# Performance work log

Measured on AMD Instinct MI355X. Metric: run time of the kernel, lower is better.

## Reference

```python
import jax, jax.numpy as jnp
import numpy as np

E = 16        # n_routed_experts
TOP_K = 2
C = 768       # n_embd
I = 1536      # intermediate_size
B, T = 8, 2048


def setup_inputs() -> dict:
    key = jax.random.key(0)
    ks = jax.random.split(key, 9)
    s = 0.02  # init scale
    return {
        "x": jax.random.normal(ks[0], (B, T, C), jnp.float32),
        "w_gate": jax.random.normal(ks[1], (C, E), jnp.float32) * s,
        "expert_bias": jnp.zeros((E,), jnp.float32),
        "wg": jax.random.normal(ks[2], (E, C, I), jnp.float32) * s,
        "wu": jax.random.normal(ks[3], (E, C, I), jnp.float32) * s,
        "wd": jax.random.normal(ks[4], (E, I, C), jnp.float32) * s,
        "swg": jax.random.normal(ks[5], (C, I), jnp.float32) * s,
        "swu": jax.random.normal(ks[6], (C, I), jnp.float32) * s,
        "swd": jax.random.normal(ks[7], (I, C), jnp.float32) * s,
    }


def _expert(x, wg_e, wu_e, wd_e):
    # SwiGLU FFN: down(silu(gate(x)) * up(x))
    return (jax.nn.silu(x @ wg_e) * (x @ wu_e)) @ wd_e


def reference(x, w_gate, expert_bias, wg, wu, wd, swg, swu, swd):
    Bq, Tq, Cq = x.shape
    xf = x.reshape(-1, Cq)  # (N, C)
    n_tok = xf.shape[0]

    # shared experts (1 expert, divided by count=1)
    shared = _expert(xf, swg, swu, swd)

    # router: softmax over (logits + bias), top-k, renormalize
    logits = xf @ w_gate + expert_bias  # (N, E)
    probs = jax.nn.softmax(logits, axis=-1)
    topk_p, topk_i = jax.lax.top_k(probs, TOP_K)
    topk_p = topk_p / jnp.sum(topk_p, axis=-1, keepdims=True)

    # combine weights per expert: zero where expert not selected
    comb = jnp.zeros((n_tok, E), xf.dtype).at[
        jnp.arange(n_tok)[:, None], topk_i
    ].add(topk_p)  # (N, E)

    routed = jnp.zeros_like(xf)
    for e in range(E):  # fixed small expert count
        routed = routed + comb[:, e:e + 1] * _expert(xf, wg[e], wu[e], wd[e])

    return (shared + routed).reshape(Bq, Tq, Cq)
```

## Files before the change

### kernel.cpp

```cpp
#include <hip/hip_runtime.h>

typedef unsigned short u16;
typedef unsigned int u32;
typedef __attribute__((ext_vector_type(4))) float f32x4;
typedef __attribute__((ext_vector_type(8))) short short8;
typedef __attribute__((ext_vector_type(4))) u16 u16x4;

#define N_TOK 16384
#define C_DIM 768
#define I_DIM 1536
#define N_EXP 16
#define TM 128
#define BK 64
#define LSTR 80
#define MAXT 400

#define CI_COUNTS 0
#define CI_STARTS 32
#define CI_NTILES 64
#define CI_TILE_E 128
#define CI_TILE_R 640
#define CI_ESLOT 2048
#define CI_SLOT 34816
#define CI_TOKW 67584
#define CI_PERM 100352

#define XB_OFF  (1u << 20)
#define ACT_OFF 26214400u
#define Y_OFF   183500800u

__device__ __forceinline__ u16 f2bf(float f) {
  u32 x = __float_as_uint(f);
  return (u16)((x + 0x7FFFu + ((x >> 16) & 1u)) >> 16);
}
__device__ __forceinline__ float bf2f(u16 h) {
  return __uint_as_float(((u32)h) << 16);
}

__global__ void router_kernel(const float* __restrict__ x, const float* __restrict__ wgate,
                              const float* __restrict__ ebias, int* __restrict__ ctrl,
                              u16* __restrict__ xb) {
  __shared__ float xs[16 * 772];
  __shared__ float wgs[C_DIM * 16];
  __shared__ float lg[16 * 16];
  int tid = threadIdx.x;
  int tok0 = blockIdx.x * 16;
  const float4* xsrc = (const float4*)(x + (size_t)tok0 * C_DIM);
  const float4* wsrc = (const float4*)wgate;
  float4* wdst = (float4*)wgs;
#pragma unroll
  for (int j = 0; j < 12; j++) {
    int q = tid + j * 256;
    float4 v = xsrc[q];
    int tk = q / 192;
    int c4 = q - tk * 192;
    *(float4*)&xs[tk * 772 + c4 * 4] = v;
    u16x4 o; o.x = f2bf(v.x); o.y = f2bf(v.y); o.z = f2bf(v.z); o.w = f2bf(v.w);
    *(u16x4*)(xb + (size_t)tok0 * C_DIM + (size_t)q * 4) = o;
    wdst[q] = wsrc[q];
  }
  __syncthreads();
  int tk = tid >> 4, e = tid & 15;
  float acc = ebias[e];
  const float* xrow = &xs[tk * 772];
  for (int c = 0; c < C_DIM; c++) acc = fmaf(xrow[c], wgs[c * 16 + e], acc);
  lg[tk * 16 + e] = acc;
  __syncthreads();
  if (tid < 16) {
    int n = tok0 + tid;
    float l0 = -1e30f, l1 = -1e30f; int i0 = 0, i1 = 0;
#pragma unroll
    for (int j = 0; j < 16; j++) {
      float l = lg[tid * 16 + j];
      if (l > l0) { l1 = l0; i1 = i0; l0 = l; i0 = j; }
      else if (l > l1) { l1 = l; i1 = j; }
    }
    float e1 = __expf(l1 - l0);
    float inv = 1.f / (1.f + e1);
    int s0 = atomicAdd(&ctrl[CI_COUNTS + i0], 1);
    int s1 = atomicAdd(&ctrl[CI_COUNTS + i1], 1);
    ctrl[CI_ESLOT + 2 * n]     = (i0 << 24) | s0;
    ctrl[CI_ESLOT + 2 * n + 1] = (i1 << 24) | s1;
    float* tw = (float*)(ctrl + CI_TOKW);
    tw[2 * n] = inv; tw[2 * n + 1] = e1 * inv;
  }
}

__global__ void tiles_kernel(int* __restrict__ ctrl) {
  if (threadIdx.x != 0) return;
  int cnt[17];
#pragma unroll
  for (int e = 0; e < 16; e++) cnt[e] = ctrl[CI_COUNTS + e];
  cnt[16] = N_TOK;
  ctrl[CI_COUNTS + 16] = N_TOK;
  int cur = 0, T = 0;
  for (int e = 0; e <= 16; e++) {
    ctrl[CI_STARTS + e] = cur;
    int nt = (cnt[e] + TM - 1) >> 7;
    for (int i = 0; i < nt; i++) {
      ctrl[CI_TILE_E + T] = e;
      ctrl[CI_TILE_R + T] = cur + i * TM;
      T++;
    }
    cur += nt << 7;
  }
  ctrl[CI_NTILES] = T;
}

__global__ void scatter_kernel(int* __restrict__ ctrl) {
  int n = blockIdx.x * 256 + threadIdx.x;
#pragma unroll
  for (int k = 0; k < 2; k++) {
    int es = ctrl[CI_ESLOT + 2 * n + k];
    int e = es >> 24;
    int slot = es & 0xFFFFFF;
    int row = ctrl[CI_STARTS + e] + slot;
    ctrl[CI_PERM + row] = n;
    ctrl[CI_SLOT + 2 * n + k] = row;
  }
}

__global__ __launch_bounds__(256, 2)
void gemm1_kernel(const u16* __restrict__ xb, const float* __restrict__ wg,
                  const float* __restrict__ wu, const float* __restrict__ swg,
                  const float* __restrict__ swu, u16* __restrict__ act,
                  const int* __restrict__ ctrl) {
  __shared__ u16 Al[TM * LSTR];
  __shared__ u16 Bg[TM * LSTR];
  __shared__ u16 Bu[TM * LSTR];
  int t = blockIdx.x;
  if (t >= ctrl[CI_NTILES]) return;
  int e = ctrl[CI_TILE_E + t];
  int row0 = ctrl[CI_TILE_R + t];
  int col0 = blockIdx.y * TM;
  int seg_start = ctrl[CI_STARTS + e];
  bool sh = (e == N_EXP);
  const float* G; const float* U;
  if (sh) { G = swg; U = swu; }
  else { G = wg + (size_t)e * C_DIM * I_DIM; U = wu + (size_t)e * C_DIM * I_DIM; }
  int row_lim = sh ? 0x7fffffff : (seg_start + ctrl[CI_COUNTS + e]);
  const int* perm = ctrl + CI_PERM;
  int tid = threadIdx.x;
  int tok[4];
#pragma unroll
  for (int j = 0; j < 4; j++) {
    int r_loc = (tid + j * 256) >> 3;
    int r = row0 + r_loc;
    tok[j] = sh ? (r - seg_start) : ((r < row_lim) ? perm[r] : 0);
  }
  f32x4 accg[4][4], accu[4][4];
#pragma unroll
  for (int m = 0; m < 4; m++)
#pragma unroll
    for (int n = 0; n < 4; n++) {
      f32x4 z = {0.f, 0.f, 0.f, 0.f};
      accg[m][n] = z; accu[m][n] = z;
    }
  int lane = tid & 63, wv = tid >> 6;
  int rh = (wv & 1) * 64, chh = (wv >> 1) * 64;
  int lr = lane & 15, lq = lane >> 4;

  for (int kk = 0; kk < C_DIM; kk += BK) {
#pragma unroll
    for (int j = 0; j < 4; j++) {
      int ch = tid + j * 256;
      int r_loc = ch >> 3;
      int c = ch & 7;
      int p = c ^ (r_loc & 7);
      float4 v = *(const float4*)(xb + (size_t)tok[j] * C_DIM + kk + c * 8);
      *(float4*)&Al[r_loc * LSTR + p * 8] = v;
    }
#pragma unroll 2
    for (int j = 0; j < 8; j++) {
      int u = tid + j * 256;
      int i = u & 127;
      int k4 = u >> 7;
      size_t gb = (size_t)(kk + k4 * 4) * I_DIM + col0 + i;
      float g0 = G[gb], g1 = G[gb + I_DIM], g2 = G[gb + 2 * I_DIM], g3 = G[gb + 3 * I_DIM];
      float h0 = U[gb], h1 = U[gb + I_DIM], h2 = U[gb + 2 * I_DIM], h3 = U[gb + 3 * I_DIM];
      int off = i * LSTR + (((k4 >> 1) ^ (i & 7)) * 8) + (k4 & 1) * 4;
      u16x4 pg; pg.x = f2bf(g0); pg.y = f2bf(g1); pg.z = f2bf(g2); pg.w = f2bf(g3);
      u16x4 pu; pu.x = f2bf(h0); pu.y = f2bf(h1); pu.z = f2bf(h2); pu.w = f2bf(h3);
      *(u16x4*)&Bg[off] = pg;
      *(u16x4*)&Bu[off] = pu;
    }
    __syncthreads();
#pragma unroll
    for (int s = 0; s < 2; s++) {
      int cidx = s * 4 + lq;
      short8 af[4], bg_[4], bu_[4];
#pragma unroll
      for (int m = 0; m < 4; m++) {
        int r = rh + m * 16 + lr;
        af[m] = *(const short8*)&Al[r * LSTR + ((cidx ^ (r & 7)) * 8)];
      }
#pragma unroll
      for (int n = 0; n < 4; n++) {
        int i = chh + n * 16 + lr;
        int off = i * LSTR + ((cidx ^ (i & 7)) * 8);
        bg_[n] = *(const short8*)&Bg[off];
        bu_[n] = *(const short8*)&Bu[off];
      }
#pragma unroll
      for (int m = 0; m < 4; m++)
#pragma unroll
        for (int n = 0; n < 4; n++) {
          accg[m][n] = __builtin_amdgcn_mfma_f32_16x16x32_bf16(af[m], bg_[n], accg[m][n], 0, 0, 0);
          accu[m][n] = __builtin_amdgcn_mfma_f32_16x16x32_bf16(af[m], bu_[n], accu[m][n], 0, 0, 0);
        }
    }
    __syncthreads();
  }
#pragma unroll
  for (int m = 0; m < 4; m++)
#pragma unroll
    for (int n = 0; n < 4; n++)
#pragma unroll
      for (int rg = 0; rg < 4; rg++) {
        float g = accg[m][n][rg];
        float h = accu[m][n][rg];
        float a = g * (1.f / (1.f + __expf(-g))) * h;
        int r_loc = rh + m * 16 + lq * 4 + rg;
        int cl = col0 + chh + n * 16 + lr;
        act[(size_t)(row0 + r_loc) * I_DIM + cl] = f2bf(a);
      }
}

__global__ __launch_bounds__(256, 2)
void gemm2_kernel(const u16* __restrict__ act, const float* __restrict__ wd,
                  const float* __restrict__ swd, u16* __restrict__ y,
                  const int* __restrict__ ctrl) {
  __shared__ u16 Al[TM * LSTR];
  __shared__ u16 Bl[TM * LSTR];
  int t = blockIdx.x;
  if (t >= ctrl[CI_NTILES]) return;
  int e = ctrl[CI_TILE_E + t];
  int row0 = ctrl[CI_TILE_R + t];
  int col0 = blockIdx.y * TM;
  const float* D = (e == N_EXP) ? swd : (wd + (size_t)e * I_DIM * C_DIM);
  int tid = threadIdx.x;
  f32x4 acc[4][4];
#pragma unroll
  for (int m = 0; m < 4; m++)
#pragma unroll
    for (int n = 0; n < 4; n++) {
      f32x4 z = {0.f, 0.f, 0.f, 0.f};
      acc[m][n] = z;
    }
  int lane = tid & 63, wv = tid >> 6;
  int rh = (wv & 1) * 64, chh = (wv >> 1) * 64;
  int lr = lane & 15, lq = lane >> 4;

  for (int kk = 0; kk < I_DIM; kk += BK) {
#pragma unroll
    for (int j = 0; j < 4; j++) {
      int ch = tid + j * 256;
      int r_loc = ch >> 3;
      int c = ch & 7;
      int p = c ^ (r_loc & 7);
      float4 v = *(const float4*)(act + (size_t)(row0 + r_loc) * I_DIM + kk + c * 8);
      *(float4*)&Al[r_loc * LSTR + p * 8] = v;
    }
#pragma unroll 2
    for (int j = 0; j < 8; j++) {
      int u = tid + j * 256;
      int i = u & 127;
      int k4 = u >> 7;
      size_t gb = (size_t)(kk + k4 * 4) * C_DIM + col0 + i;
      float g0 = D[gb], g1 = D[gb + C_DIM], g2 = D[gb + 2 * C_DIM], g3 = D[gb + 3 * C_DIM];
      int off = i * LSTR + (((k4 >> 1) ^ (i & 7)) * 8) + (k4 & 1) * 4;
      u16x4 pg; pg.x = f2bf(g0); pg.y = f2bf(g1); pg.z = f2bf(g2); pg.w = f2bf(g3);
      *(u16x4*)&Bl[off] = pg;
    }
    __syncthreads();
#pragma unroll
    for (int s = 0; s < 2; s++) {
      int cidx = s * 4 + lq;
      short8 af[4], bf_[4];
#pragma unroll
      for (int m = 0; m < 4; m++) {
        int r = rh + m * 16 + lr;
        af[m] = *(const short8*)&Al[r * LSTR + ((cidx ^ (r & 7)) * 8)];
      }
#pragma unroll
      for (int n = 0; n < 4; n++) {
        int i = chh + n * 16 + lr;
        bf_[n] = *(const short8*)&Bl[i * LSTR + ((cidx ^ (i & 7)) * 8)];
      }
#pragma unroll
      for (int m = 0; m < 4; m++)
#pragma unroll
        for (int n = 0; n < 4; n++)
          acc[m][n] = __builtin_amdgcn_mfma_f32_16x16x32_bf16(af[m], bf_[n], acc[m][n], 0, 0, 0);
    }
    __syncthreads();
  }
#pragma unroll
  for (int m = 0; m < 4; m++)
#pragma unroll
    for (int n = 0; n < 4; n++)
#pragma unroll
      for (int rg = 0; rg < 4; rg++) {
        int r_loc = rh + m * 16 + lq * 4 + rg;
        int cl = col0 + chh + n * 16 + lr;
        y[(size_t)(row0 + r_loc) * C_DIM + cl] = f2bf(acc[m][n][rg]);
      }
}

__global__ void combine_kernel(const u16* __restrict__ y, const int* __restrict__ ctrl,
                               float* __restrict__ out) {
  int idx = blockIdx.x * 256 + threadIdx.x;
  int n = idx / 192;
  int c = (idx - n * 192) * 4;
  int srow = ctrl[CI_STARTS + 16] + n;
  int s0 = ctrl[CI_SLOT + 2 * n];
  int s1 = ctrl[CI_SLOT + 2 * n + 1];
  const float* tw = (const float*)(ctrl + CI_TOKW);
  float w0 = tw[2 * n], w1 = tw[2 * n + 1];
  u16x4 a = *(const u16x4*)(y + (size_t)srow * C_DIM + c);
  u16x4 b = *(const u16x4*)(y + (size_t)s0 * C_DIM + c);
  u16x4 d = *(const u16x4*)(y + (size_t)s1 * C_DIM + c);
  float4 o;
  o.x = bf2f(a.x) + w0 * bf2f(b.x) + w1 * bf2f(d.x);
  o.y = bf2f(a.y) + w0 * bf2f(b.y) + w1 * bf2f(d.y);
  o.z = bf2f(a.z) + w0 * bf2f(b.z) + w1 * bf2f(d.z);
  o.w = bf2f(a.w) + w0 * bf2f(b.w) + w1 * bf2f(d.w);
  *(float4*)(out + (size_t)idx * 4) = o;
}

extern "C" void kernel_launch(void* const* d_in, const int* in_sizes, int n_in,
                              void* d_out, int out_size, void* d_ws, size_t ws_size,
                              hipStream_t stream) {
  (void)in_sizes; (void)n_in; (void)out_size; (void)ws_size;
  const float* x     = (const float*)d_in[0];
  const float* wgate = (const float*)d_in[1];
  const float* ebias = (const float*)d_in[2];
  const float* wg    = (const float*)d_in[3];
  const float* wu    = (const float*)d_in[4];
  const float* wd    = (const float*)d_in[5];
  const float* swg   = (const float*)d_in[6];
  const float* swu   = (const float*)d_in[7];
  const float* swd   = (const float*)d_in[8];
  float* out = (float*)d_out;
  char* ws = (char*)d_ws;
  int* ctrl = (int*)ws;
  u16* xb  = (u16*)(ws + XB_OFF);
  u16* act = (u16*)(ws + ACT_OFF);
  u16* y   = (u16*)(ws + Y_OFF);

  hipMemsetAsync(ws, 0, 256, stream);
  router_kernel<<<N_TOK / 16, 256, 0, stream>>>(x, wgate, ebias, ctrl, xb);
  tiles_kernel<<<1, 64, 0, stream>>>(ctrl);
  scatter_kernel<<<N_TOK / 256, 256, 0, stream>>>(ctrl);
  gemm1_kernel<<<dim3(MAXT, I_DIM / TM), 256, 0, stream>>>(xb, wg, wu, swg, swu, act, ctrl);
  gemm2_kernel<<<dim3(MAXT, C_DIM / TM), 256, 0, stream>>>(act, wd, swd, y, ctrl);
  combine_kernel<<<(N_TOK * C_DIM / 4) / 256, 256, 0, stream>>>(y, ctrl, out);
}
```

Measured before the change: 1.181 ms.

## Pre-convert weights to bf16, DMA tiles into LDS, fuse combine via atomics

A new convert kernel transposes and converts all expert and shared weights to bf16 once per call. The GEMMs then load A and B tiles straight into LDS with global_load_lds 16-byte DMA instead of doing per-element fp32 loads and conversion in registers. gemm2 scatters weighted results directly into the output with atomicAdd, which removes the y buffer and the combine kernel. The GEMMs run in two passes so the act buffer is smaller and may stay cache-resident, and the router gets a transposed, vectorized dot product. In exchange it adds a full weight-conversion pass on every call, output memsets, and many fp32 atomics, and the atomics make the summation order nondeterministic.

```diff
diff --git a/kernel.cpp b/kernel.cpp
--- a/kernel.cpp
+++ b/kernel.cpp
@@ -5,6 +5,7 @@
 typedef __attribute__((ext_vector_type(4))) float f32x4;
 typedef __attribute__((ext_vector_type(8))) short short8;
 typedef __attribute__((ext_vector_type(4))) u16 u16x4;
+typedef __attribute__((ext_vector_type(8))) u16 u16x8;
 
 #define N_TOK 16384
 #define C_DIM 768
@@ -12,22 +13,22 @@
 #define N_EXP 16
 #define TM 128
 #define BK 64
-#define LSTR 80
 #define MAXT 400
+#define PASS_T 200
 
 #define CI_COUNTS 0
 #define CI_STARTS 32
 #define CI_NTILES 64
 #define CI_TILE_E 128
-#define CI_TILE_R 640
 #define CI_ESLOT 2048
-#define CI_SLOT 34816
-#define CI_TOKW 67584
-#define CI_PERM 100352
-
-#define XB_OFF  (1u << 20)
-#define ACT_OFF 26214400u
-#define Y_OFF   183500800u
+#define CI_TOKW 36864
+#define CI_PERM 102400
+#define CI_RW 153600
+
+#define XB_OFF  1048576u
+#define WGU_OFF 26214400u
+#define WDP_OFF 106430464u
+#define ACT_OFF 146538496u
 
 __device__ __forceinline__ u16 f2bf(float f) {
   u32 x = __float_as_uint(f);
@@ -35,19 +36,57 @@
 }
 __device__ __forceinline__ float bf2f(u16 h) {
   return __uint_as_float(((u32)h) << 16);
+}
+__device__ __forceinline__ void dma16(const void* g, void* l) {
+  __builtin_amdgcn_global_load_lds(
+      (const __attribute__((address_space(1))) unsigned int*)g,
+      (__attribute__((address_space(3))) unsigned int*)l, 16, 0, 0);
+}
+
+__global__ void convert_kernel(const float* __restrict__ wg, const float* __restrict__ wu,
+                               const float* __restrict__ wd, const float* __restrict__ swg,
+                               const float* __restrict__ swu, const float* __restrict__ swd,
+                               u16* __restrict__ wgu, u16* __restrict__ wdp) {
+  int bid = blockIdx.x;
+  const float* src; u16* dst; int K, N, base_n;
+  if (bid < 34 * 48) {
+    int m = bid / 48, nb = bid % 48;
+    int e = m >> 1, gu = m & 1;
+    src = (e < N_EXP) ? ((gu ? wu : wg) + (size_t)e * C_DIM * I_DIM) : (gu ? swu : swg);
+    dst = wgu + (size_t)m * (C_DIM * I_DIM);
+    K = C_DIM; N = I_DIM; base_n = nb * 32;
+  } else {
+    int b2 = bid - 34 * 48;
+    int e = b2 / 24, nb = b2 % 24;
+    src = (e < N_EXP) ? (wd + (size_t)e * I_DIM * C_DIM) : swd;
+    dst = wdp + (size_t)e * (I_DIM * C_DIM);
+    K = I_DIM; N = C_DIM; base_n = nb * 32;
+  }
+  int tid = threadIdx.x, lane = tid & 63, wv = tid >> 6;
+  int lsub = lane >> 3, lchk = lane & 7;
+  int ng = base_n + wv * 8 + lsub;
+  int c = lchk ^ (ng & 7);
+  const float* s0 = src + ng;
+  u16* drow = dst + (size_t)ng * K;
+  for (int k0 = 0; k0 < K; k0 += 64) {
+    u16x8 o;
+#pragma unroll
+    for (int j = 0; j < 8; j++)
+      o[j] = f2bf(s0[(size_t)(k0 + c * 8 + j) * N]);
+    *(u16x8*)&drow[k0 + lchk * 8] = o;
+  }
 }
 
 __global__ void router_kernel(const float* __restrict__ x, const float* __restrict__ wgate,
                               const float* __restrict__ ebias, int* __restrict__ ctrl,
                               u16* __restrict__ xb) {
   __shared__ float xs[16 * 772];
-  __shared__ float wgs[C_DIM * 16];
+  __shared__ float wgsT[16 * 772];
   __shared__ float lg[16 * 16];
   int tid = threadIdx.x;
   int tok0 = blockIdx.x * 16;
   const float4* xsrc = (const float4*)(x + (size_t)tok0 * C_DIM);
   const float4* wsrc = (const float4*)wgate;
-  float4* wdst = (float4*)wgs;
 #pragma unroll
   for (int j = 0; j < 12; j++) {
     int q = tid + j * 256;
@@ -57,13 +96,23 @@
     *(float4*)&xs[tk * 772 + c4 * 4] = v;
     u16x4 o; o.x = f2bf(v.x); o.y = f2bf(v.y); o.z = f2bf(v.z); o.w = f2bf(v.w);
     *(u16x4*)(xb + (size_t)tok0 * C_DIM + (size_t)q * 4) = o;
-    wdst[q] = wsrc[q];
+    float4 w = wsrc[q];
+    int c = q >> 2, e0 = (q & 3) * 4;
+    wgsT[(e0 + 0) * 772 + c] = w.x;
+    wgsT[(e0 + 1) * 772 + c] = w.y;
+    wgsT[(e0 + 2) * 772 + c] = w.z;
+    wgsT[(e0 + 3) * 772 + c] = w.w;
   }
   __syncthreads();
   int tk = tid >> 4, e = tid & 15;
   float acc = ebias[e];
-  const float* xrow = &xs[tk * 772];
-  for (int c = 0; c < C_DIM; c++) acc = fmaf(xrow[c], wgs[c * 16 + e], acc);
+  const float4* xr = (const float4*)&xs[tk * 772];
+  const float4* wr = (const float4*)&wgsT[e * 772];
+#pragma unroll 4
+  for (int c4 = 0; c4 < 192; c4++) {
+    float4 xv = xr[c4], wv = wr[c4];
+    acc = fmaf(xv.x, wv.x, fmaf(xv.y, wv.y, fmaf(xv.z, wv.z, fmaf(xv.w, wv.w, acc))));
+  }
   lg[tk * 16 + e] = acc;
   __syncthreads();
   if (tid < 16) {
@@ -97,11 +146,7 @@
   for (int e = 0; e <= 16; e++) {
     ctrl[CI_STARTS + e] = cur;
     int nt = (cnt[e] + TM - 1) >> 7;
-    for (int i = 0; i < nt; i++) {
-      ctrl[CI_TILE_E + T] = e;
-      ctrl[CI_TILE_R + T] = cur + i * TM;
-      T++;
-    }
+    for (int i = 0; i < nt; i++) ctrl[CI_TILE_E + T++] = e;
     cur += nt << 7;
   }
   ctrl[CI_NTILES] = T;
@@ -109,6 +154,8 @@
 
 __global__ void scatter_kernel(int* __restrict__ ctrl) {
   int n = blockIdx.x * 256 + threadIdx.x;
+  const float* tw = (const float*)(ctrl + CI_TOKW);
+  float* rw = (float*)(ctrl + CI_RW);
 #pragma unroll
   for (int k = 0; k < 2; k++) {
     int es = ctrl[CI_ESLOT + 2 * n + k];
@@ -116,38 +163,46 @@
     int slot = es & 0xFFFFFF;
     int row = ctrl[CI_STARTS + e] + slot;
     ctrl[CI_PERM + row] = n;
-    ctrl[CI_SLOT + 2 * n + k] = row;
-  }
+    rw[row] = tw[2 * n + k];
+  }
+  int srow = ctrl[CI_STARTS + 16] + n;
+  ctrl[CI_PERM + srow] = n;
+  rw[srow] = 1.0f;
 }
 
 __global__ __launch_bounds__(256, 2)
-void gemm1_kernel(const u16* __restrict__ xb, const float* __restrict__ wg,
-                  const float* __restrict__ wu, const float* __restrict__ swg,
-                  const float* __restrict__ swu, u16* __restrict__ act,
-                  const int* __restrict__ ctrl) {
-  __shared__ u16 Al[TM * LSTR];
-  __shared__ u16 Bg[TM * LSTR];
-  __shared__ u16 Bu[TM * LSTR];
-  int t = blockIdx.x;
+void gemm1_kernel(const u16* __restrict__ xb, const u16* __restrict__ wgu,
+                  u16* __restrict__ act, const int* __restrict__ ctrl, int tile0) {
+  __shared__ u16 Al[TM * BK];
+  __shared__ u16 Bg[TM * BK];
+  __shared__ u16 Bu[TM * BK];
+  int t = tile0 + blockIdx.x;
   if (t >= ctrl[CI_NTILES]) return;
   int e = ctrl[CI_TILE_E + t];
-  int row0 = ctrl[CI_TILE_R + t];
+  int row0 = t << 7;
+  int row0l = blockIdx.x << 7;
   int col0 = blockIdx.y * TM;
   int seg_start = ctrl[CI_STARTS + e];
   bool sh = (e == N_EXP);
-  const float* G; const float* U;
-  if (sh) { G = swg; U = swu; }
-  else { G = wg + (size_t)e * C_DIM * I_DIM; U = wu + (size_t)e * C_DIM * I_DIM; }
+  const u16* G = wgu + (size_t)(2 * e) * (C_DIM * I_DIM);
+  const u16* U = G + C_DIM * I_DIM;
   int row_lim = sh ? 0x7fffffff : (seg_start + ctrl[CI_COUNTS + e]);
   const int* perm = ctrl + CI_PERM;
   int tid = threadIdx.x;
-  int tok[4];
+  int lane = tid & 63, wv = tid >> 6;
+  int lsub = lane >> 3;
+  int lchk = lane & 7;
+  int co = (lchk ^ lsub) * 8;
+  const u16* aptr[4];
 #pragma unroll
   for (int j = 0; j < 4; j++) {
-    int r_loc = (tid + j * 256) >> 3;
-    int r = row0 + r_loc;
-    tok[j] = sh ? (r - seg_start) : ((r < row_lim) ? perm[r] : 0);
-  }
+    int r = row0 + wv * 32 + j * 8 + lsub;
+    int tok = sh ? (r - seg_start) : ((r < row_lim) ? perm[r] : 0);
+    aptr[j] = xb + (size_t)tok * C_DIM + co;
+  }
+  size_t boff = (size_t)(col0 + wv * 32 + lsub) * C_DIM + lchk * 8;
+  int ldst = wv * 2048;
+
   f32x4 accg[4][4], accu[4][4];
 #pragma unroll
   for (int m = 0; m < 4; m++)
@@ -156,33 +211,15 @@
       f32x4 z = {0.f, 0.f, 0.f, 0.f};
       accg[m][n] = z; accu[m][n] = z;
     }
-  int lane = tid & 63, wv = tid >> 6;
+  int lr = lane & 15, lq = lane >> 4;
   int rh = (wv & 1) * 64, chh = (wv >> 1) * 64;
-  int lr = lane & 15, lq = lane >> 4;
 
   for (int kk = 0; kk < C_DIM; kk += BK) {
 #pragma unroll
     for (int j = 0; j < 4; j++) {
-      int ch = tid + j * 256;
-      int r_loc = ch >> 3;
-      int c = ch & 7;
-      int p = c ^ (r_loc & 7);
-      float4 v = *(const float4*)(xb + (size_t)tok[j] * C_DIM + kk + c * 8);
-      *(float4*)&Al[r_loc * LSTR + p * 8] = v;
-    }
-#pragma unroll 2
-    for (int j = 0; j < 8; j++) {
-      int u = tid + j * 256;
-      int i = u & 127;
-      int k4 = u >> 7;
-      size_t gb = (size_t)(kk + k4 * 4) * I_DIM + col0 + i;
-      float g0 = G[gb], g1 = G[gb + I_DIM], g2 = G[gb + 2 * I_DIM], g3 = G[gb + 3 * I_DIM];
-      float h0 = U[gb], h1 = U[gb + I_DIM], h2 = U[gb + 2 * I_DIM], h3 = U[gb + 3 * I_DIM];
-      int off = i * LSTR + (((k4 >> 1) ^ (i & 7)) * 8) + (k4 & 1) * 4;
-      u16x4 pg; pg.x = f2bf(g0); pg.y = f2bf(g1); pg.z = f2bf(g2); pg.w = f2bf(g3);
-      u16x4 pu; pu.x = f2bf(h0); pu.y = f2bf(h1); pu.z = f2bf(h2); pu.w = f2bf(h3);
-      *(u16x4*)&Bg[off] = pg;
-      *(u16x4*)&Bu[off] = pu;
+      dma16(aptr[j] + kk,                    Al + ldst + j * 512);
+      dma16(G + boff + j * (8 * C_DIM) + kk, Bg + ldst + j * 512);
+      dma16(U + boff + j * (8 * C_DIM) + kk, Bu + ldst + j * 512);
     }
     __syncthreads();
 #pragma unroll
@@ -192,12 +229,12 @@
 #pragma unroll
       for (int m = 0; m < 4; m++) {
         int r = rh + m * 16 + lr;
-        af[m] = *(const short8*)&Al[r * LSTR + ((cidx ^ (r & 7)) * 8)];
+        af[m] = *(const short8*)&Al[r * 64 + ((cidx ^ (r & 7)) * 8)];
       }
 #pragma unroll
       for (int n = 0; n < 4; n++) {
         int i = chh + n * 16 + lr;
-        int off = i * LSTR + ((cidx ^ (i & 7)) * 8);
+        int off = i * 64 + ((cidx ^ (i & 7)) * 8);
         bg_[n] = *(const short8*)&Bg[off];
         bu_[n] = *(const short8*)&Bu[off];
       }
@@ -222,23 +259,30 @@
         float a = g * (1.f / (1.f + __expf(-g))) * h;
         int r_loc = rh + m * 16 + lq * 4 + rg;
         int cl = col0 + chh + n * 16 + lr;
-        act[(size_t)(row0 + r_loc) * I_DIM + cl] = f2bf(a);
-      }
-}
-
-__global__ __launch_bounds__(256, 2)
-void gemm2_kernel(const u16* __restrict__ act, const float* __restrict__ wd,
-                  const float* __restrict__ swd, u16* __restrict__ y,
-                  const int* __restrict__ ctrl) {
-  __shared__ u16 Al[TM * LSTR];
-  __shared__ u16 Bl[TM * LSTR];
-  int t = blockIdx.x;
+        act[(size_t)(row0l + r_loc) * I_DIM + cl] = f2bf(a);
+      }
+}
+
+__global__ __launch_bounds__(256, 3)
+void gemm2_kernel(const u16* __restrict__ act, const u16* __restrict__ wdp,
+                  float* __restrict__ out, const int* __restrict__ ctrl, int tile0) {
+  __shared__ u16 Al[TM * BK];
+  __shared__ u16 Bl[TM * BK];
+  int t = tile0 + blockIdx.x;
   if (t >= ctrl[CI_NTILES]) return;
   int e = ctrl[CI_TILE_E + t];
-  int row0 = ctrl[CI_TILE_R + t];
+  int row0 = t << 7;
+  int row0l = blockIdx.x << 7;
   int col0 = blockIdx.y * TM;
-  const float* D = (e == N_EXP) ? swd : (wd + (size_t)e * I_DIM * C_DIM);
+  const u16* D = wdp + (size_t)e * (I_DIM * C_DIM);
   int tid = threadIdx.x;
+  int lane = tid & 63, wv = tid >> 6;
+  int lsub = lane >> 3, lchk = lane & 7;
+  int co = (lchk ^ lsub) * 8;
+  const u16* abase = act + (size_t)(row0l + wv * 32 + lsub) * I_DIM + co;
+  size_t boff = (size_t)(col0 + wv * 32 + lsub) * I_DIM + lchk * 8;
+  int ldst = wv * 2048;
+
   f32x4 acc[4][4];
 #pragma unroll
   for (int m = 0; m < 4; m++)
@@ -247,30 +291,14 @@
       f32x4 z = {0.f, 0.f, 0.f, 0.f};
       acc[m][n] = z;
     }
-  int lane = tid & 63, wv = tid >> 6;
+  int lr = lane & 15, lq = lane >> 4;
   int rh = (wv & 1) * 64, chh = (wv >> 1) * 64;
-  int lr = lane & 15, lq = lane >> 4;
 
   for (int kk = 0; kk < I_DIM; kk += BK) {
 #pragma unroll
     for (int j = 0; j < 4; j++) {
-      int ch = tid + j * 256;
-      int r_loc = ch >> 3;
-      int c = ch & 7;
-      int p = c ^ (r_loc & 7);
-      float4 v = *(const float4*)(act + (size_t)(row0 + r_loc) * I_DIM + kk + c * 8);
-      *(float4*)&Al[r_loc * LSTR + p * 8] = v;
-    }
-#pragma unroll 2
-    for (int j = 0; j < 8; j++) {
-      int u = tid + j * 256;
-      int i = u & 127;
-      int k4 = u >> 7;
-      size_t gb = (size_t)(kk + k4 * 4) * C_DIM + col0 + i;
-      float g0 = D[gb], g1 = D[gb + C_DIM], g2 = D[gb + 2 * C_DIM], g3 = D[gb + 3 * C_DIM];
-      int off = i * LSTR + (((k4 >> 1) ^ (i & 7)) * 8) + (k4 & 1) * 4;
-      u16x4 pg; pg.x = f2bf(g0); pg.y = f2bf(g1); pg.z = f2bf(g2); pg.w = f2bf(g3);
-      *(u16x4*)&Bl[off] = pg;
+      dma16(abase + (size_t)j * 8 * I_DIM + kk, Al + ldst + j * 512);
+      dma16(D + boff + j * (8 * I_DIM) + kk,    Bl + ldst + j * 512);
     }
     __syncthreads();
 #pragma unroll
@@ -280,12 +308,12 @@
 #pragma unroll
       for (int m = 0; m < 4; m++) {
         int r = rh + m * 16 + lr;
-        af[m] = *(const short8*)&Al[r * LSTR + ((cidx ^ (r & 7)) * 8)];
+        af[m] = *(const short8*)&Al[r * 64 + ((cidx ^ (r & 7)) * 8)];
       }
 #pragma unroll
       for (int n = 0; n < 4; n++) {
         int i = chh + n * 16 + lr;
-        bf_[n] = *(const short8*)&Bl[i * LSTR + ((cidx ^ (i & 7)) * 8)];
+        bf_[n] = *(const short8*)&Bl[i * 64 + ((cidx ^ (i & 7)) * 8)];
       }
 #pragma unroll
       for (int m = 0; m < 4; m++)
@@ -295,37 +323,21 @@
     }
     __syncthreads();
   }
+  const int* perm = ctrl + CI_PERM;
+  const float* rw = (const float*)(ctrl + CI_RW);
 #pragma unroll
   for (int m = 0; m < 4; m++)
 #pragma unroll
-    for (int n = 0; n < 4; n++)
-#pragma unroll
-      for (int rg = 0; rg < 4; rg++) {
-        int r_loc = rh + m * 16 + lq * 4 + rg;
-        int cl = col0 + chh + n * 16 + lr;
-        y[(size_t)(row0 + r_loc) * C_DIM + cl] = f2bf(acc[m][n][rg]);
-      }
-}
-
-__global__ void combine_kernel(const u16* __restrict__ y, const int* __restrict__ ctrl,
-                               float* __restrict__ out) {
-  int idx = blockIdx.x * 256 + threadIdx.x;
-  int n = idx / 192;
-  int c = (idx - n * 192) * 4;
-  int srow = ctrl[CI_STARTS + 16] + n;
-  int s0 = ctrl[CI_SLOT + 2 * n];
-  int s1 = ctrl[CI_SLOT + 2 * n + 1];
-  const float* tw = (const float*)(ctrl + CI_TOKW);
-  float w0 = tw[2 * n], w1 = tw[2 * n + 1];
-  u16x4 a = *(const u16x4*)(y + (size_t)srow * C_DIM + c);
-  u16x4 b = *(const u16x4*)(y + (size_t)s0 * C_DIM + c);
-  u16x4 d = *(const u16x4*)(y + (size_t)s1 * C_DIM + c);
-  float4 o;
-  o.x = bf2f(a.x) + w0 * bf2f(b.x) + w1 * bf2f(d.x);
-  o.y = bf2f(a.y) + w0 * bf2f(b.y) + w1 * bf2f(d.y);
-  o.z = bf2f(a.z) + w0 * bf2f(b.z) + w1 * bf2f(d.z);
-  o.w = bf2f(a.w) + w0 * bf2f(b.w) + w1 * bf2f(d.w);
-  *(float4*)(out + (size_t)idx * 4) = o;
+    for (int rg = 0; rg < 4; rg++) {
+      int rgrow = row0 + rh + m * 16 + lq * 4 + rg;
+      int tokn = perm[rgrow];
+      if (tokn < 0) continue;
+      float w = rw[rgrow];
+      float* obase = out + (size_t)tokn * C_DIM + col0 + chh + lr;
+#pragma unroll
+      for (int n = 0; n < 4; n++)
+        atomicAdd(obase + n * 16, acc[m][n][rg] * w);
+    }
 }
 
 extern "C" void kernel_launch(void* const* d_in, const int* in_sizes, int n_in,
@@ -345,14 +357,19 @@
   char* ws = (char*)d_ws;
   int* ctrl = (int*)ws;
   u16* xb  = (u16*)(ws + XB_OFF);
+  u16* wgu = (u16*)(ws + WGU_OFF);
+  u16* wdp = (u16*)(ws + WDP_OFF);
   u16* act = (u16*)(ws + ACT_OFF);
-  u16* y   = (u16*)(ws + Y_OFF);
 
   hipMemsetAsync(ws, 0, 256, stream);
+  hipMemsetAsync(ws + (size_t)CI_PERM * 4, 0xFF, 51200 * 4, stream);
+  hipMemsetAsync(d_out, 0, (size_t)N_TOK * C_DIM * 4, stream);
   router_kernel<<<N_TOK / 16, 256, 0, stream>>>(x, wgate, ebias, ctrl, xb);
   tiles_kernel<<<1, 64, 0, stream>>>(ctrl);
   scatter_kernel<<<N_TOK / 256, 256, 0, stream>>>(ctrl);
-  gemm1_kernel<<<dim3(MAXT, I_DIM / TM), 256, 0, stream>>>(xb, wg, wu, swg, swu, act, ctrl);
-  gemm2_kernel<<<dim3(MAXT, C_DIM / TM), 256, 0, stream>>>(act, wd, swd, y, ctrl);
-  combine_kernel<<<(N_TOK * C_DIM / 4) / 256, 256, 0, stream>>>(y, ctrl, out);
-}
+  convert_kernel<<<34 * 48 + 17 * 24, 256, 0, stream>>>(wg, wu, wd, swg, swu, swd, wgu, wdp);
+  for (int p = 0; p < 2; p++) {
+    gemm1_kernel<<<dim3(PASS_T, I_DIM / TM), 256, 0, stream>>>(xb, wgu, act, ctrl, p * PASS_T);
+    gemm2_kernel<<<dim3(PASS_T, C_DIM / TM), 256, 0, stream>>>(act, wdp, out, ctrl, p * PASS_T);
+  }
+}
```

Measured after the change: 1.018 ms. 13.8% less time.
